# Optimization experiments

Measured on AMD Instinct MI355X. Metric: run time of the kernel, lower is better.

The kernel has to match this reference:

```python
import jax, jax.numpy as jnp
import numpy as np

N = 50000
E = 500000
NODE_F = 128
POS_F = 3
COORD_F = 64
EDGE_IN = 2 * NODE_F + 1  # 257


def _linear_params(key, fan_in, fan_out):
    k1, k2 = jax.random.split(key)
    bound = 1.0 / np.sqrt(fan_in)
    W = jax.random.uniform(k1, (fan_in, fan_out), jnp.float32, -bound, bound)
    b = jax.random.uniform(k2, (fan_out,), jnp.float32, -bound, bound)
    return W, b


def setup_inputs() -> dict:
    key = jax.random.key(0)
    ks = jax.random.split(key, 8)
    x = jax.random.normal(ks[0], (N, NODE_F + POS_F), jnp.float32)
    edge_index = jax.random.randint(ks[1], (2, E), 0, N, jnp.int64)
    W_e1, b_e1 = _linear_params(ks[2], EDGE_IN, 2 * EDGE_IN)
    W_e2, b_e2 = _linear_params(ks[3], 2 * EDGE_IN, COORD_F)
    W_c1, b_c1 = _linear_params(ks[4], COORD_F, 4 * COORD_F)
    W_c2, b_c2 = _linear_params(ks[5], 4 * COORD_F, 1)
    W_n1, b_n1 = _linear_params(ks[6], NODE_F + COORD_F, 2 * NODE_F)
    W_n2, b_n2 = _linear_params(ks[7], 2 * NODE_F, NODE_F)
    return {"x": x, "edge_index": edge_index,
            "W_e1": W_e1, "b_e1": b_e1, "W_e2": W_e2, "b_e2": b_e2,
            "W_c1": W_c1, "b_c1": b_c1, "W_c2": W_c2, "b_c2": b_c2,
            "W_n1": W_n1, "b_n1": b_n1, "W_n2": W_n2, "b_n2": b_n2}


def reference(x, edge_index, W_e1, b_e1, W_e2, b_e2, W_c1, b_c1, W_c2, b_c2,
              W_n1, b_n1, W_n2, b_n2):
    node = x[:, :-POS_F]            # (N, 128)
    coords = x[:, -POS_F:]          # (N, 3)
    src = edge_index[0]             # j (source)
    dst = edge_index[1]             # i (target)

    rel_coords = coords[src] - coords[dst]                          # (E, 3)
    rel_dist = jnp.sqrt(jnp.sum(rel_coords ** 2, -1, keepdims=True))  # (E, 1)

    # message: edge_mlp(cat[x_i, x_j, edge_attr])
    e_in = jnp.concatenate([node[dst], node[src], rel_dist], axis=-1)  # (E, 257)
    h = jax.nn.silu(e_in @ W_e1 + b_e1)
    m_ij = jax.nn.silu(h @ W_e2 + b_e2)                             # (E, 64)
    coord_w = jax.nn.silu(m_ij @ W_c1 + b_c1) @ W_c2 + b_c2         # (E, 1)

    # scatter-sum aggregation to target nodes
    m_i = jax.ops.segment_sum(m_ij, dst, num_segments=N)            # (N, 64)
    w_i = jax.ops.segment_sum(coord_w, dst, num_segments=N)         # (N, 1)
    r_i = jax.ops.segment_sum(rel_coords, dst, num_segments=N)      # (N, 3)

    coords_out = coords + w_i * r_i
    n_in = jnp.concatenate([node, m_i], axis=-1)                    # (N, 192)
    hidden = jax.nn.silu(n_in @ W_n1 + b_n1) @ W_n2 + b_n2 + node   # (N, 128)
    return jnp.concatenate([hidden, coords_out], axis=-1)           # (N, 131)
```

## Files before the change

### kernel.cpp

```cpp
#include <hip/hip_runtime.h>
#include <hip/hip_bf16.h>
#include <hip/hip_fp16.h>

#define NN 50000
#define NE 500000
#define DCAP 48

using bf16x8 = __attribute__((ext_vector_type(8))) short;
using f16x8  = __attribute__((ext_vector_type(8))) _Float16;
using f32x4  = __attribute__((ext_vector_type(4))) float;
using f32x2  = __attribute__((ext_vector_type(2))) float;

__device__ __forceinline__ float b2f(unsigned short s) {
  union { unsigned u; float f; } v; v.u = ((unsigned)s) << 16; return v.f;
}
__device__ __forceinline__ unsigned short f2b(float f) {
  __hip_bfloat16 h = __float2bfloat16(f);
  return *reinterpret_cast<unsigned short*>(&h);
}
__device__ __forceinline__ unsigned short f2h(float f) {
  __half h = __float2half(f);
  return *reinterpret_cast<unsigned short*>(&h);
}
__device__ __forceinline__ float hu2f(unsigned short s) {
  __half h; *reinterpret_cast<unsigned short*>(&h) = s; return __half2float(h);
}
__device__ __forceinline__ unsigned pack2(float a, float b) {
  __hip_bfloat162 h = __float22bfloat162_rn(make_float2(a, b));
  return *reinterpret_cast<unsigned*>(&h);
}
__device__ __forceinline__ unsigned pack2h(float a, float b) {
  __half2 h = __float22half2_rn(make_float2(a, b));
  return *reinterpret_cast<unsigned*>(&h);
}
__device__ __forceinline__ __half2 h2u(unsigned u) {
  union { unsigned v; __half2 h; } x; x.v = u; return x.h;
}
__device__ __forceinline__ unsigned u2h(__half2 h) {
  union { __half2 h; unsigned v; } x; x.h = h; return x.v;
}
__device__ __forceinline__ float silu_f(float x) {
  return x * __builtin_amdgcn_rcpf(1.f + __expf(-x));
}
__device__ __forceinline__ __half2 silu2(__half2 z) {
  const __half2 one = __float2half2_rn(1.f);
  __half2 e = h2exp(__hneg2(z));
  return __hmul2(z, h2rcp(__hadd2(e, one)));
}

#define WPREP 269344
__global__ void prep_all(const float* __restrict__ we1,
                         const float* __restrict__ be1,
                         const float* __restrict__ we2,
                         const float* __restrict__ be2,
                         const float* __restrict__ wc1,
                         const float* __restrict__ wn1,
                         const float* __restrict__ wn2,
                         const float* __restrict__ x,
                         unsigned short* __restrict__ A1p,
                         unsigned short* __restrict__ A2p,
                         unsigned short* __restrict__ AdB,
                         unsigned short* __restrict__ W2p,
                         unsigned short* __restrict__ Wc1p,
                         unsigned short* __restrict__ Wn1p,
                         unsigned short* __restrict__ Wn2p,
                         float* __restrict__ be1p,
                         unsigned short* __restrict__ node_p,
                         float* __restrict__ coords_p) {
  int i = blockIdx.x * 256 + threadIdx.x;
  if (i < 67584) {
    int n = i / 128, k = i % 128;
    A1p[i] = (n < 514) ? f2b(we1[k * 514 + n]) : (unsigned short)0;
  } else if (i < 135168) {
    int j = i - 67584; int n = j / 128, k = j % 128;
    A2p[j] = (n < 514) ? f2b(we1[(128 + k) * 514 + n]) : (unsigned short)0;
  } else if (i < 135696) {
    int j = i - 135168;
    AdB[j] = (j < 514) ? f2h(we1[256 * 514 + j]) : (unsigned short)0;
  } else if (i < 170512) {
    int j = i - 135696; int n = j / 544, lk = j % 544;
    unsigned short v = 0;
    if (lk < 514) v = f2h(we2[lk * 64 + n]);
    else if (lk == 514) v = f2h(be2[n]);
    W2p[j] = v;
  } else if (i < 186896) {
    int j = i - 170512; int n = j / 64, k = j % 64;
    Wc1p[j] = f2b(wc1[k * 256 + n]);
  } else if (i < 236048) {
    int j = i - 186896; int n = j / 192, k = j % 192;
    Wn1p[j] = f2b(wn1[k * 256 + n]);
  } else if (i < 268816) {
    int j = i - 236048; int n = j / 256, k = j % 256;
    Wn2p[j] = f2b(wn2[k * 128 + n]);
  } else if (i < WPREP) {
    int j = i - 268816;
    be1p[j] = (j < 514) ? be1[j] : 0.f;
  } else {
    int j = i - WPREP;
    if (j < NN * 16) {
      int g = j >> 4, c = j & 15;
      const float* s = x + g * 131 + c * 8;
      unsigned short* d = node_p + g * 128 + c * 8;
#pragma unroll
      for (int q = 0; q < 8; q++) d[q] = f2b(s[q]);
    } else if (j < NN * 17) {
      int g = j - NN * 16;
      float4 c;
      c.x = x[g * 131 + 128];
      c.y = x[g * 131 + 129];
      c.z = x[g * 131 + 130];
      c.w = 0.f;
      *(float4*)(coords_p + g * 4) = c;
    }
  }
}

__global__ void build_adj(const int* __restrict__ eidx,
                          int* __restrict__ cnt, int* __restrict__ adj) {
  int e = blockIdx.x * 256 + threadIdx.x;
  if (e < NE) {
    int d = eidx[NE + e];
    d = min(max(d, 0), NN - 1);
    int slot = atomicAdd(&cnt[d], 1);
    if (slot < DCAP) adj[d * DCAP + slot] = e;
  }
}

__global__ void assign_off(const int* __restrict__ cnt,
                           int* __restrict__ off,
                           int* __restrict__ total) {
  int g = blockIdx.x * 256 + threadIdx.x;
  int lane = threadIdx.x & 63;
  int deg = (g < NN) ? min(cnt[g], DCAP) : 0;
  int incl = deg;
#pragma unroll
  for (int d = 1; d < 64; d <<= 1) {
    int v = __shfl_up(incl, d, 64);
    if (lane >= d) incl += v;
  }
  int wsum = __shfl(incl, 63, 64);
  int base = 0;
  if (lane == 63) base = atomicAdd(total, wsum);
  base = __shfl(base, 63, 64);
  if (g < NN) off[g] = base + incl - deg;
}

__global__ void compact_adj(const int* __restrict__ cnt,
                            const int* __restrict__ off,
                            const int* __restrict__ adj,
                            const int* __restrict__ eidx,
                            int* __restrict__ eord,
                            int* __restrict__ esrc) {
  int t = blockIdx.x * 256 + threadIdx.x;
  if (t >= NN * DCAP) return;
  int g = t / DCAP, k = t % DCAP;
  int deg = min(cnt[g], DCAP);
  if (k >= deg) return;
  int e = adj[t];
  int o = off[g] + k;
  eord[o] = e;
  int s = eidx[e];
  esrc[o] = min(max(s, 0), NN - 1);
}

__launch_bounds__(256, 2)
__global__ void pgemm_kernel(const unsigned short* __restrict__ node_p,
                             const unsigned short* __restrict__ A1p,
                             const unsigned short* __restrict__ A2p,
                             const float* __restrict__ be1p,
                             unsigned short* __restrict__ P1,
                             unsigned char* __restrict__ P2) {
  __shared__ unsigned short sNode[64][136];
  int tid = threadIdx.x, blk = blockIdx.x;
  int lane = tid & 63, wv = tid >> 6, l16 = lane & 15, quad = lane >> 4;
#pragma unroll
  for (int it = 0; it < 4; it++) {
    int t = tid + it * 256;
    int row = t >> 4, ch = t & 15;
    int g = blk * 64 + row;
    if (g >= NN) g = 0;
    *(bf16x8*)(&sNode[row][ch * 8]) = *(const bf16x8*)(node_p + g * 128 + ch * 8);
  }
  __syncthreads();
#pragma unroll 1
  for (int t = 0; t < 9; t++) {
    int T = wv + 4 * t;
    if (T >= 33) break;
    f32x4 a1[4], a2[4];
#pragma unroll
    for (int s = 0; s < 4; s++) {
      a1[s] = (f32x4){0.f, 0.f, 0.f, 0.f};
      a2[s] = (f32x4){0.f, 0.f, 0.f, 0.f};
    }
    for (int kb = 0; kb < 4; kb++) {
      bf16x8 b1 = *(const bf16x8*)(A1p + (T * 16 + l16) * 128 + kb * 32 + quad * 8);
      bf16x8 b2 = *(const bf16x8*)(A2p + (T * 16 + l16) * 128 + kb * 32 + quad * 8);
#pragma unroll
      for (int s = 0; s < 4; s++) {
        bf16x8 a = *(const bf16x8*)(&sNode[s * 16 + l16][kb * 32 + quad * 8]);
        a1[s] = __builtin_amdgcn_mfma_f32_16x16x32_bf16(b1, a, a1[s], 0, 0, 0);
        a2[s] = __builtin_amdgcn_mfma_f32_16x16x32_bf16(b2, a, a2[s], 0, 0, 0);
      }
    }
    int nb = T * 16 + quad * 4;
    float4 b4 = *(const float4*)(be1p + nb);
    bool v0 = nb + 0 < 514, v1 = nb + 1 < 514, v2 = nb + 2 < 514, v3 = nb + 3 < 514;
#pragma unroll
    for (int s = 0; s < 4; s++) {
      int g = blk * 64 + s * 16 + l16;
      if (g < NN) {
        float p0 = v0 ? a1[s][0] + b4.x : 0.f;
        float p1v = v1 ? a1[s][1] + b4.y : 0.f;
        float p2v = v2 ? a1[s][2] + b4.z : 0.f;
        float p3 = v3 ? a1[s][3] + b4.w : 0.f;
        *(uint2*)(P1 + g * 528 + nb) = make_uint2(pack2h(p0, p1v), pack2h(p2v, p3));
        float q0 = v0 ? a2[s][0] : 0.f;
        float q1 = v1 ? a2[s][1] : 0.f;
        float q2 = v2 ? a2[s][2] : 0.f;
        float q3 = v3 ? a2[s][3] : 0.f;
        int w8 = __builtin_amdgcn_cvt_pk_fp8_f32(q0, q1, 0, false);
        w8 = __builtin_amdgcn_cvt_pk_fp8_f32(q2, q3, w8, true);
        *(unsigned*)(P2 + g * 528 + nb) = (unsigned)w8;
      }
    }
  }
}

__launch_bounds__(256, 3)
__global__ void edge_kernel(const unsigned short* __restrict__ P1,
                            const unsigned char* __restrict__ P2,
                            const unsigned short* __restrict__ AdB,
                            const float* __restrict__ coords_p,
                            const int* __restrict__ eidx,
                            const int* __restrict__ eord,
                            const unsigned short* __restrict__ W2p,
                            const unsigned short* __restrict__ Wc1p,
                            const float* __restrict__ bc1,
                            const float* __restrict__ bc2,
                            const float* __restrict__ wc2,
                            unsigned short* __restrict__ medge,
                            float* __restrict__ coordw) {
  __shared__ unsigned short sHc[48][168];
  __shared__ unsigned short sM[48][72];
  __shared__ int sDst[48];
  __shared__ int sSrc[48];
  __shared__ int sE[48];
  __shared__ float sDistF[48];
  __shared__ float sCwPart[4][48];
  int tid = threadIdx.x, blk = blockIdx.x;
  int lane = tid & 63, wv = tid >> 6, l16 = lane & 15, quad = lane >> 4;

  unsigned tailP1 = 0u, tailP2 = 0u;
  if (tid < 48) {
    int r = blk * 48 + tid;
    int e = (r < NE) ? eord[r] : -1;
    sE[tid] = e;
    if (e < 0) e = 0;
    int s = eidx[e], d = eidx[NE + e];
    s = min(max(s, 0), NN - 1);
    d = min(max(d, 0), NN - 1);
    float4 cs = *(const float4*)(coords_p + s * 4);
    float4 cd = *(const float4*)(coords_p + d * 4);
    float rx = cs.x - cd.x, ry = cs.y - cd.y, rz = cs.z - cd.z;
    sDst[tid] = d;
    sSrc[tid] = s;
    sDistF[tid] = sqrtf(rx * rx + ry * ry + rz * rz);
    tailP1 = *(const unsigned*)(P1 + d * 528 + 512);
    tailP2 = *(const unsigned*)(P2 + s * 528 + 512);
  }
  __syncthreads();

  int cg = tid & 15, er = tid >> 4;
  const unsigned short* p1b[3];
  const unsigned char* p2b[3];
  __half2 d2[3];
#pragma unroll
  for (int it = 0; it < 3; it++) {
    int edge = er + it * 16;
    p1b[it] = P1 + sDst[edge] * 528 + cg * 8;
    p2b[it] = P2 + sSrc[edge] * 528 + cg * 8;
    d2[it] = __float2half2_rn(sDistF[edge]);
  }
  const unsigned short* adB = AdB + cg * 8;
  const unsigned short* w2b = W2p + (wv * 16 + l16) * 544 + quad * 8;

  uint2 u2r[4][3];
#pragma unroll
  for (int ch = 0; ch < 4; ch++)
#pragma unroll
    for (int it = 0; it < 3; it++)
      u2r[ch][it] = *(const uint2*)(p2b[it] + ch * 128);

  f32x4 macc[3];
#pragma unroll
  for (int s = 0; s < 3; s++) macc[s] = (f32x4){0.f, 0.f, 0.f, 0.f};

#pragma unroll
  for (int ch = 0; ch < 4; ch++) {
    uint4 uva = *(const uint4*)(adB + ch * 128);
    __half2 va0 = h2u(uva.x), va1 = h2u(uva.y), va2 = h2u(uva.z), va3 = h2u(uva.w);
#pragma unroll
    for (int it = 0; it < 3; it++) {
      int edge = er + it * 16;
      uint4 u1 = *(const uint4*)(p1b[it] + ch * 128);
      uint2 u2 = u2r[ch][it];
      f32x2 c0 = __builtin_amdgcn_cvt_pk_f32_fp8((int)u2.x, false);
      f32x2 c1 = __builtin_amdgcn_cvt_pk_f32_fp8((int)u2.x, true);
      f32x2 c2 = __builtin_amdgcn_cvt_pk_f32_fp8((int)u2.y, false);
      f32x2 c3 = __builtin_amdgcn_cvt_pk_f32_fp8((int)u2.y, true);
      __half2 q0 = h2u(pack2h(c0.x, c0.y));
      __half2 q1 = h2u(pack2h(c1.x, c1.y));
      __half2 q2 = h2u(pack2h(c2.x, c2.y));
      __half2 q3 = h2u(pack2h(c3.x, c3.y));
      __half2 z0 = __hfma2(va0, d2[it], __hadd2(h2u(u1.x), q0));
      __half2 z1 = __hfma2(va1, d2[it], __hadd2(h2u(u1.y), q1));
      __half2 z2 = __hfma2(va2, d2[it], __hadd2(h2u(u1.z), q2));
      __half2 z3 = __hfma2(va3, d2[it], __hadd2(h2u(u1.w), q3));
      *(uint4*)(&sHc[edge][cg * 8]) = make_uint4(
          u2h(silu2(z0)), u2h(silu2(z1)), u2h(silu2(z2)), u2h(silu2(z3)));
    }
    if (ch == 3 && tid < 48) {
      float dist = sDistF[tid];
      __half2 hp1 = h2u(tailP1);
      f32x2 t2 = __builtin_amdgcn_cvt_pk_f32_fp8((int)tailP2, false);
      float h512 = silu_f(__low2float(hp1) + t2.x + dist * hu2f(AdB[512]));
      float h513 = silu_f(__high2float(hp1) + t2.y + dist * hu2f(AdB[513]));
      *(uint4*)(&sHc[tid][128]) = make_uint4(pack2h(h512, h513), pack2h(1.0f, 0.f), 0u, 0u);
      *(uint4*)(&sHc[tid][136]) = make_uint4(0u, 0u, 0u, 0u);
      *(uint4*)(&sHc[tid][144]) = make_uint4(0u, 0u, 0u, 0u);
      *(uint4*)(&sHc[tid][152]) = make_uint4(0u, 0u, 0u, 0u);
    }
    __syncthreads();
    const int nkb = (ch == 3) ? 5 : 4;
#pragma unroll
    for (int kb = 0; kb < nkb; kb++) {
      f16x8 b = *(const f16x8*)(w2b + ch * 128 + kb * 32);
#pragma unroll
      for (int s = 0; s < 3; s++) {
        f16x8 a = *(const f16x8*)(&sHc[s * 16 + l16][kb * 32 + quad * 8]);
        macc[s] = __builtin_amdgcn_mfma_f32_16x16x32_f16(b, a, macc[s], 0, 0, 0);
      }
    }
    __syncthreads();
  }

  {
    int nb = wv * 16 + quad * 4;
#pragma unroll
    for (int s = 0; s < 3; s++) {
      unsigned lo = pack2(silu_f(macc[s][0]), silu_f(macc[s][1]));
      unsigned hi = pack2(silu_f(macc[s][2]), silu_f(macc[s][3]));
      *(uint2*)(&sM[s * 16 + l16][nb]) = make_uint2(lo, hi);
    }
  }
  __syncthreads();

  {
    float cw[3] = {0.f, 0.f, 0.f};
#pragma unroll
    for (int jt = 0; jt < 4; jt++) {
      int T = wv * 4 + jt;
      f32x4 cacc[3];
#pragma unroll
      for (int s = 0; s < 3; s++) cacc[s] = (f32x4){0.f, 0.f, 0.f, 0.f};
#pragma unroll
      for (int kb = 0; kb < 2; kb++) {
        bf16x8 b = *(const bf16x8*)(Wc1p + (T * 16 + l16) * 64 + kb * 32 + quad * 8);
#pragma unroll
        for (int s = 0; s < 3; s++) {
          bf16x8 a = *(const bf16x8*)(&sM[s * 16 + l16][kb * 32 + quad * 8]);
          cacc[s] = __builtin_amdgcn_mfma_f32_16x16x32_bf16(b, a, cacc[s], 0, 0, 0);
        }
      }
      int nb = T * 16 + quad * 4;
      float4 b4 = *(const float4*)(bc1 + nb);
      float4 w4 = *(const float4*)(wc2 + nb);
#pragma unroll
      for (int s = 0; s < 3; s++) {
        cw[s] += silu_f(cacc[s][0] + b4.x) * w4.x;
        cw[s] += silu_f(cacc[s][1] + b4.y) * w4.y;
        cw[s] += silu_f(cacc[s][2] + b4.z) * w4.z;
        cw[s] += silu_f(cacc[s][3] + b4.w) * w4.w;
      }
    }
#pragma unroll
    for (int s = 0; s < 3; s++) {
      cw[s] += __shfl_xor(cw[s], 16, 64);
      cw[s] += __shfl_xor(cw[s], 32, 64);
    }
    if (quad == 0) {
#pragma unroll
      for (int s = 0; s < 3; s++) sCwPart[wv][s * 16 + l16] = cw[s];
    }
  }
  __syncthreads();
#pragma unroll
  for (int it = 0; it < 2; it++) {
    int idx = it * 256 + tid;
    if (idx < 384) {
      int row = idx >> 3, ch8 = idx & 7;
      int r = blk * 48 + row;
      if (r < NE && sE[row] >= 0)
        *(bf16x8*)(medge + (size_t)r * 64 + ch8 * 8) = *(const bf16x8*)(&sM[row][ch8 * 8]);
    }
  }
  if (tid < 48) {
    int r = blk * 48 + tid;
    if (r < NE && sE[tid] >= 0) {
      float v = sCwPart[0][tid] + sCwPart[1][tid] + sCwPart[2][tid] + sCwPart[3][tid]
                + bc2[0];
      coordw[r] = v;
    }
  }
}

__launch_bounds__(256, 2)
__global__ void node_mlp_kernel(const unsigned short* __restrict__ node_p,
                                const float* __restrict__ x,
                                const float* __restrict__ coords_p,
                                const unsigned short* __restrict__ medge,
                                const float* __restrict__ coordw,
                                const int* __restrict__ esrc,
                                const int* __restrict__ cnt,
                                const int* __restrict__ off,
                                const unsigned short* __restrict__ Wn1p,
                                const unsigned short* __restrict__ Wn2p,
                                const float* __restrict__ bn1,
                                const float* __restrict__ bn2,
                                float* __restrict__ out) {
  __shared__ unsigned short sNin[64][200];
  __shared__ unsigned short sHid[64][264];
  __shared__ float sWr[64][4];
  int tid = threadIdx.x, blk = blockIdx.x;
  int lane = tid & 63, wv = tid >> 6, l16 = lane & 15, quad = lane >> 4;

#pragma unroll
  for (int it = 0; it < 4; it++) {
    int t = tid + it * 256;
    int row = t >> 4, ch = t & 15;
    int g = blk * 64 + row;
    if (g >= NN) g = 0;
    *(bf16x8*)(&sNin[row][ch * 8]) = *(const bf16x8*)(node_p + g * 128 + ch * 8);
  }
  {
    int row = tid >> 2, c = tid & 3;
    int g = blk * 64 + row;
    int gg = (g < NN) ? g : 0;
    int deg = min(cnt[gg], DCAP);
    int o = off[gg];
    float acc[16];
#pragma unroll
    for (int i = 0; i < 16; i++) acc[i] = 0.f;
    float sc = 0.f;
    float cgc = (c < 3) ? coords_p[gg * 4 + c] : 0.f;
    for (int k = 0; k < deg; k++) {
      int r = o + k;
      const unsigned short* mrow = medge + (size_t)r * 64 + c * 16;
      bf16x8 a0 = *(const bf16x8*)(mrow);
      bf16x8 a1 = *(const bf16x8*)(mrow + 8);
#pragma unroll
      for (int i = 0; i < 8; i++) acc[i] += b2f((unsigned short)a0[i]);
#pragma unroll
      for (int i = 0; i < 8; i++) acc[8 + i] += b2f((unsigned short)a1[i]);
      if (c == 3) {
        sc += coordw[r];
      } else {
        int s = esrc[r];
        sc += coords_p[s * 4 + c] - cgc;
      }
    }
    unsigned u[8];
#pragma unroll
    for (int i = 0; i < 8; i++) u[i] = pack2(acc[2 * i], acc[2 * i + 1]);
    *(uint4*)(&sNin[row][128 + c * 16]) = make_uint4(u[0], u[1], u[2], u[3]);
    *(uint4*)(&sNin[row][128 + c * 16 + 8]) = make_uint4(u[4], u[5], u[6], u[7]);
    sWr[row][c] = sc;
  }
  __syncthreads();
  {
    f32x4 acc[4][4];
#pragma unroll
    for (int j = 0; j < 4; j++)
#pragma unroll
      for (int s = 0; s < 4; s++) acc[j][s] = (f32x4){0.f, 0.f, 0.f, 0.f};
    for (int kb = 0; kb < 6; kb++) {
      bf16x8 afr[4], bfr[4];
#pragma unroll
      for (int s = 0; s < 4; s++)
        afr[s] = *(const bf16x8*)(&sNin[s * 16 + l16][kb * 32 + quad * 8]);
#pragma unroll
      for (int j = 0; j < 4; j++)
        bfr[j] = *(const bf16x8*)(Wn1p + ((wv * 4 + j) * 16 + l16) * 192 + kb * 32 + quad * 8);
#pragma unroll
      for (int j = 0; j < 4; j++)
#pragma unroll
        for (int s = 0; s < 4; s++)
          acc[j][s] = __builtin_amdgcn_mfma_f32_16x16x32_bf16(bfr[j], afr[s], acc[j][s], 0, 0, 0);
    }
#pragma unroll
    for (int j = 0; j < 4; j++) {
      int nb = (wv * 4 + j) * 16 + quad * 4;
      float4 b4 = *(const float4*)(bn1 + nb);
#pragma unroll
      for (int s = 0; s < 4; s++) {
        unsigned lo = pack2(silu_f(acc[j][s][0] + b4.x), silu_f(acc[j][s][1] + b4.y));
        unsigned hi = pack2(silu_f(acc[j][s][2] + b4.z), silu_f(acc[j][s][3] + b4.w));
        *(uint2*)(&sHid[s * 16 + l16][nb]) = make_uint2(lo, hi);
      }
    }
  }
  __syncthreads();
  {
    f32x4 acc[2][4];
#pragma unroll
    for (int j = 0; j < 2; j++)
#pragma unroll
      for (int s = 0; s < 4; s++) acc[j][s] = (f32x4){0.f, 0.f, 0.f, 0.f};
    for (int kb = 0; kb < 8; kb++) {
      bf16x8 afr[4], bfr[2];
#pragma unroll
      for (int s = 0; s < 4; s++)
        afr[s] = *(const bf16x8*)(&sHid[s * 16 + l16][kb * 32 + quad * 8]);
#pragma unroll
      for (int j = 0; j < 2; j++)
        bfr[j] = *(const bf16x8*)(Wn2p + ((wv * 2 + j) * 16 + l16) * 256 + kb * 32 + quad * 8);
#pragma unroll
      for (int j = 0; j < 2; j++)
#pragma unroll
        for (int s = 0; s < 4; s++)
          acc[j][s] = __builtin_amdgcn_mfma_f32_16x16x32_bf16(bfr[j], afr[s], acc[j][s], 0, 0, 0);
    }
#pragma unroll
    for (int j = 0; j < 2; j++) {
      int nb = (wv * 2 + j) * 16 + quad * 4;
      float4 b4 = *(const float4*)(bn2 + nb);
#pragma unroll
      for (int s = 0; s < 4; s++) {
        int g = blk * 64 + s * 16 + l16;
        if (g < NN) {
          int base = g * 131 + nb;
          out[base + 0] = acc[j][s][0] + b4.x + x[base + 0];
          out[base + 1] = acc[j][s][1] + b4.y + x[base + 1];
          out[base + 2] = acc[j][s][2] + b4.z + x[base + 2];
          out[base + 3] = acc[j][s][3] + b4.w + x[base + 3];
        }
      }
    }
  }
  if (tid < 64) {
    int g = blk * 64 + tid;
    if (g < NN) {
      float w = sWr[tid][3];
      out[g * 131 + 128] = coords_p[g * 4 + 0] + w * sWr[tid][0];
      out[g * 131 + 129] = coords_p[g * 4 + 1] + w * sWr[tid][1];
      out[g * 131 + 130] = coords_p[g * 4 + 2] + w * sWr[tid][2];
    }
  }
}

extern "C" void kernel_launch(void* const* d_in, const int* in_sizes, int n_in,
                              void* d_out, int out_size, void* d_ws, size_t ws_size,
                              hipStream_t stream) {
  const float* x   = (const float*)d_in[0];
  const int* eidx  = (const int*)d_in[1];
  const float* we1 = (const float*)d_in[2];
  const float* be1 = (const float*)d_in[3];
  const float* we2 = (const float*)d_in[4];
  const float* be2 = (const float*)d_in[5];
  const float* wc1 = (const float*)d_in[6];
  const float* bc1 = (const float*)d_in[7];
  const float* wc2 = (const float*)d_in[8];
  const float* bc2 = (const float*)d_in[9];
  const float* wn1 = (const float*)d_in[10];
  const float* bn1 = (const float*)d_in[11];
  const float* wn2 = (const float*)d_in[12];
  const float* bn2 = (const float*)d_in[13];

  char* ws = (char*)d_ws;
  unsigned short* A1p    = (unsigned short*)(ws + 0);
  unsigned short* A2p    = (unsigned short*)(ws + 135168);
  unsigned short* AdB    = (unsigned short*)(ws + 270336);
  unsigned short* W2p    = (unsigned short*)(ws + 271392);
  unsigned short* Wc1p   = (unsigned short*)(ws + 341024);
  unsigned short* Wn1p   = (unsigned short*)(ws + 373792);
  unsigned short* Wn2p   = (unsigned short*)(ws + 472096);
  float* be1p            = (float*)(ws + 537632);
  unsigned short* node_p = (unsigned short*)(ws + 539744);
  float* coords_p        = (float*)(ws + 13339744);
  unsigned short* medge  = (unsigned short*)(ws + 14139744);
  float* coordw          = (float*)(ws + 78139744);
  int* cnt               = (int*)(ws + 80139744);
  int* adj               = (int*)(ws + 80339744);
  unsigned short* P1     = (unsigned short*)(ws + 103539744);
  unsigned char* P2      = (unsigned char*)(ws + 156339744);
  int* off               = (int*)(ws + 209139744);
  int* eord              = (int*)(ws + 209339748);
  int* esrc              = (int*)(ws + 211339748);
  int* total             = (int*)(ws + 213339748);

  hipMemsetAsync(cnt, 0, NN * sizeof(int), stream);
  hipMemsetAsync(total, 0, sizeof(int), stream);
  hipMemsetAsync(eord, 0xFF, NE * sizeof(int), stream);
  prep_all<<<(WPREP + NN * 17 + 255) / 256, 256, 0, stream>>>(
      we1, be1, we2, be2, wc1, wn1, wn2, x,
      A1p, A2p, AdB, W2p, Wc1p, Wn1p, Wn2p, be1p, node_p, coords_p);
  pgemm_kernel<<<(NN + 63) / 64, 256, 0, stream>>>(node_p, A1p, A2p, be1p, P1, P2);
  build_adj<<<(NE + 255) / 256, 256, 0, stream>>>(eidx, cnt, adj);
  assign_off<<<(NN + 255) / 256, 256, 0, stream>>>(cnt, off, total);
  compact_adj<<<(NN * DCAP + 255) / 256, 256, 0, stream>>>(cnt, off, adj, eidx,
                                                           eord, esrc);
  edge_kernel<<<(NE + 47) / 48, 256, 0, stream>>>(P1, P2, AdB, coords_p, eidx, eord,
                                                  W2p, Wc1p, bc1, bc2, wc2,
                                                  medge, coordw);
  node_mlp_kernel<<<(NN + 63) / 64, 256, 0, stream>>>(node_p, x, coords_p, medge,
                                                      coordw, esrc, cnt, off,
                                                      Wn1p, Wn2p, bn1, bn2,
                                                      (float*)d_out);
}
```

Measured before the change: 447.5 us.

## Precompute per-edge relative coords in compaction and fold memsets into prep kernel

The three hipMemsetAsync calls are replaced by extra threads in prep_all, so cnt, total and esrc are cleared inside the existing launch. compact_adj now writes the source index, destination node, and a float4 of relative coords plus distance for each sorted edge. The edge kernel and node MLP kernel read these precomputed arrays instead of doing eidx and coords gathers. This cuts random gathers in the downstream kernels but adds a 16-byte-per-edge scoord buffer write and read.

Result: faster. 425.2 us (-5.0%).

```diff
diff --git a/kernel.cpp b/kernel.cpp
--- a/kernel.cpp
+++ b/kernel.cpp
@@ -49,6 +49,10 @@
 }
 
 #define WPREP 269344
+#define B0 (WPREP + NN * 17)
+#define B1 (B0 + NN)
+#define B2 (B1 + 1)
+#define PREP_TOTAL (B2 + NE)
 __global__ void prep_all(const float* __restrict__ we1,
                          const float* __restrict__ be1,
                          const float* __restrict__ we2,
@@ -66,7 +70,10 @@
                          unsigned short* __restrict__ Wn2p,
                          float* __restrict__ be1p,
                          unsigned short* __restrict__ node_p,
-                         float* __restrict__ coords_p) {
+                         float* __restrict__ coords_p,
+                         int* __restrict__ cnt,
+                         int* __restrict__ total,
+                         int* __restrict__ esrc) {
   int i = blockIdx.x * 256 + threadIdx.x;
   if (i < 67584) {
     int n = i / 128, k = i % 128;
@@ -95,7 +102,7 @@
   } else if (i < WPREP) {
     int j = i - 268816;
     be1p[j] = (j < 514) ? be1[j] : 0.f;
-  } else {
+  } else if (i < B0) {
     int j = i - WPREP;
     if (j < NN * 16) {
       int g = j >> 4, c = j & 15;
@@ -103,7 +110,7 @@
       unsigned short* d = node_p + g * 128 + c * 8;
 #pragma unroll
       for (int q = 0; q < 8; q++) d[q] = f2b(s[q]);
-    } else if (j < NN * 17) {
+    } else {
       int g = j - NN * 16;
       float4 c;
       c.x = x[g * 131 + 128];
@@ -112,6 +119,12 @@
       c.w = 0.f;
       *(float4*)(coords_p + g * 4) = c;
     }
+  } else if (i < B1) {
+    cnt[i - B0] = 0;
+  } else if (i < B2) {
+    total[0] = 0;
+  } else if (i < PREP_TOTAL) {
+    esrc[i - B2] = -1;
   }
 }
 
@@ -149,18 +162,28 @@
                             const int* __restrict__ off,
                             const int* __restrict__ adj,
                             const int* __restrict__ eidx,
-                            int* __restrict__ eord,
-                            int* __restrict__ esrc) {
+                            const float* __restrict__ coords_p,
+                            int* __restrict__ esrc,
+                            int* __restrict__ edst,
+                            float* __restrict__ scoord) {
   int t = blockIdx.x * 256 + threadIdx.x;
   if (t >= NN * DCAP) return;
   int g = t / DCAP, k = t % DCAP;
   int deg = min(cnt[g], DCAP);
   if (k >= deg) return;
   int e = adj[t];
+  int s = eidx[e];
+  s = min(max(s, 0), NN - 1);
   int o = off[g] + k;
-  eord[o] = e;
-  int s = eidx[e];
-  esrc[o] = min(max(s, 0), NN - 1);
+  esrc[o] = s;
+  edst[o] = g;
+  float4 cs = *(const float4*)(coords_p + s * 4);
+  float4 cd = *(const float4*)(coords_p + g * 4);
+  float rx = cs.x - cd.x, ry = cs.y - cd.y, rz = cs.z - cd.z;
+  float4 sc;
+  sc.x = rx; sc.y = ry; sc.z = rz;
+  sc.w = sqrtf(rx * rx + ry * ry + rz * rz);
+  *(float4*)(scoord + (size_t)o * 4) = sc;
 }
 
 __launch_bounds__(256, 2)
@@ -230,9 +253,9 @@
 __global__ void edge_kernel(const unsigned short* __restrict__ P1,
                             const unsigned char* __restrict__ P2,
                             const unsigned short* __restrict__ AdB,
-                            const float* __restrict__ coords_p,
-                            const int* __restrict__ eidx,
-                            const int* __restrict__ eord,
+                            const int* __restrict__ esrcA,
+                            const int* __restrict__ edstA,
+                            const float* __restrict__ scoord,
                             const unsigned short* __restrict__ W2p,
                             const unsigned short* __restrict__ Wc1p,
                             const float* __restrict__ bc1,
@@ -253,20 +276,21 @@
   unsigned tailP1 = 0u, tailP2 = 0u;
   if (tid < 48) {
     int r = blk * 48 + tid;
-    int e = (r < NE) ? eord[r] : -1;
-    sE[tid] = e;
-    if (e < 0) e = 0;
-    int s = eidx[e], d = eidx[NE + e];
-    s = min(max(s, 0), NN - 1);
-    d = min(max(d, 0), NN - 1);
-    float4 cs = *(const float4*)(coords_p + s * 4);
-    float4 cd = *(const float4*)(coords_p + d * 4);
-    float rx = cs.x - cd.x, ry = cs.y - cd.y, rz = cs.z - cd.z;
+    int s = (r < NE) ? esrcA[r] : -1;
+    sE[tid] = s;
+    int ss = (s < 0) ? 0 : s;
+    int d = 0;
+    float dist = 0.f;
+    if (s >= 0) {
+      d = edstA[r];
+      d = min(max(d, 0), NN - 1);
+      dist = scoord[(size_t)r * 4 + 3];
+    }
     sDst[tid] = d;
-    sSrc[tid] = s;
-    sDistF[tid] = sqrtf(rx * rx + ry * ry + rz * rz);
+    sSrc[tid] = ss;
+    sDistF[tid] = dist;
     tailP1 = *(const unsigned*)(P1 + d * 528 + 512);
-    tailP2 = *(const unsigned*)(P2 + s * 528 + 512);
+    tailP2 = *(const unsigned*)(P2 + ss * 528 + 512);
   }
   __syncthreads();
 
@@ -420,7 +444,7 @@
                                 const float* __restrict__ coords_p,
                                 const unsigned short* __restrict__ medge,
                                 const float* __restrict__ coordw,
-                                const int* __restrict__ esrc,
+                                const float* __restrict__ scoord,
                                 const int* __restrict__ cnt,
                                 const int* __restrict__ off,
                                 const unsigned short* __restrict__ Wn1p,
@@ -452,7 +476,6 @@
 #pragma unroll
     for (int i = 0; i < 16; i++) acc[i] = 0.f;
     float sc = 0.f;
-    float cgc = (c < 3) ? coords_p[gg * 4 + c] : 0.f;
     for (int k = 0; k < deg; k++) {
       int r = o + k;
       const unsigned short* mrow = medge + (size_t)r * 64 + c * 16;
@@ -462,12 +485,7 @@
       for (int i = 0; i < 8; i++) acc[i] += b2f((unsigned short)a0[i]);
 #pragma unroll
       for (int i = 0; i < 8; i++) acc[8 + i] += b2f((unsigned short)a1[i]);
-      if (c == 3) {
-        sc += coordw[r];
-      } else {
-        int s = esrc[r];
-        sc += coords_p[s * 4 + c] - cgc;
-      }
+      sc += (c == 3) ? coordw[r] : scoord[(size_t)r * 4 + c];
     }
     unsigned u[8];
 #pragma unroll
@@ -594,26 +612,26 @@
   unsigned short* P1     = (unsigned short*)(ws + 103539744);
   unsigned char* P2      = (unsigned char*)(ws + 156339744);
   int* off               = (int*)(ws + 209139744);
-  int* eord              = (int*)(ws + 209339748);
+  int* edst              = (int*)(ws + 209339748);
   int* esrc              = (int*)(ws + 211339748);
   int* total             = (int*)(ws + 213339748);
-
-  hipMemsetAsync(cnt, 0, NN * sizeof(int), stream);
-  hipMemsetAsync(total, 0, sizeof(int), stream);
-  hipMemsetAsync(eord, 0xFF, NE * sizeof(int), stream);
-  prep_all<<<(WPREP + NN * 17 + 255) / 256, 256, 0, stream>>>(
+  float* scoord          = (float*)(ws + 213339760);
+
+  prep_all<<<(PREP_TOTAL + 255) / 256, 256, 0, stream>>>(
       we1, be1, we2, be2, wc1, wn1, wn2, x,
-      A1p, A2p, AdB, W2p, Wc1p, Wn1p, Wn2p, be1p, node_p, coords_p);
+      A1p, A2p, AdB, W2p, Wc1p, Wn1p, Wn2p, be1p, node_p, coords_p,
+      cnt, total, esrc);
   pgemm_kernel<<<(NN + 63) / 64, 256, 0, stream>>>(node_p, A1p, A2p, be1p, P1, P2);
   build_adj<<<(NE + 255) / 256, 256, 0, stream>>>(eidx, cnt, adj);
   assign_off<<<(NN + 255) / 256, 256, 0, stream>>>(cnt, off, total);
   compact_adj<<<(NN * DCAP + 255) / 256, 256, 0, stream>>>(cnt, off, adj, eidx,
-                                                           eord, esrc);
-  edge_kernel<<<(NE + 47) / 48, 256, 0, stream>>>(P1, P2, AdB, coords_p, eidx, eord,
+                                                           coords_p, esrc, edst,
+                                                           scoord);
+  edge_kernel<<<(NE + 47) / 48, 256, 0, stream>>>(P1, P2, AdB, esrc, edst, scoord,
                                                   W2p, Wc1p, bc1, bc2, wc2,
                                                   medge, coordw);
   node_mlp_kernel<<<(NN + 63) / 64, 256, 0, stream>>>(node_p, x, coords_p, medge,
-                                                      coordw, esrc, cnt, off,
+                                                      coordw, scoord, cnt, off,
                                                       Wn1p, Wn2p, bn1, bn2,
                                                       (float*)d_out);
 }
```
